# Optimization experiments

Measured on AMD Instinct MI355X. Metric: run time of the kernel, lower is better.

Reference implementation:

```python
import jax, jax.numpy as jnp
import numpy as np

SIDE = 9
STATE = SIDE * SIDE          # 81
NA = 5                       # stay, up, down, left, right
_MOVES = [(0, 0), (-1, 0), (1, 0), (0, -1), (0, 1)]

def _dest(s, a):
    r, c = divmod(s, SIDE)
    nr, nc = r + _MOVES[a][0], c + _MOVES[a][1]
    if 0 <= nr < SIDE and 0 <= nc < SIDE:
        return nr * SIDE + nc
    return s  # off-grid moves stay in place

# inflows[i] = all (s, a) with dest(s, a) == i; flattened as edge lists.
_src, _dst = [], []
for s in range(STATE):
    for a in range(NA):
        _src.append(s * NA + a)          # flat index into action_count[B, 81*5]
        _dst.append(_dest(s, a))
INFLOW_SRC = jnp.asarray(np.array(_src, dtype=np.int32))
INFLOW_DST = jnp.asarray(np.array(_dst, dtype=np.int32))


def setup_inputs() -> dict:
    key = jax.random.key(0)
    k1, k2, k3, k4, k5 = jax.random.split(key, 5)
    B = 131072
    obs = jax.random.uniform(k1, (B, 3 * STATE), dtype=jnp.float32)
    action_count = jax.random.uniform(k2, (B, STATE, NA), dtype=jnp.float32)
    W1 = jax.random.normal(k3, (STATE, 32), dtype=jnp.float32) * 0.1
    W2 = jax.random.normal(k4, (32, 32), dtype=jnp.float32) * 0.1
    W3 = jax.random.normal(k5, (32, 1), dtype=jnp.float32) * 0.1
    b3 = jnp.zeros((1,), dtype=jnp.float32)
    return {"obs": obs, "action_count": action_count,
            "W1": W1, "W2": W2, "W3": W3, "b3": b3}


def reference(obs, action_count, W1, W2, W3, b3):
    B = obs.shape[0]
    demand_count = obs[:, 2 * STATE:]                       # [B, 81]
    af = action_count.reshape(B, STATE * NA)                # [B, 405]
    # Vectorized replacement of the per-state gather+stack+reduce_sum loops:
    # next_state_count[b, i] = sum over (s,a) in inflows[i] of action_count[b, s, a]
    next_state_count = jnp.zeros((B, STATE), af.dtype).at[:, INFLOW_DST].add(af[:, INFLOW_SRC])
    # served_demand[b, i] = min(next_state_count[b, i], demand_count[b, i])
    served_demands = jnp.minimum(next_state_count, demand_count)
    immediate_reward = jnp.sum(served_demands, axis=1)      # [B]
    # value MLP on next_state_count (hidden dense layers have no bias)
    x = jax.nn.relu(next_state_count @ W1)
    x = jax.nn.relu(x @ W2)
    next_return = (x @ W3 + b3)[:, 0]                       # [B]
    symbolic_val = immediate_reward + next_return           # stack+reduce_sum
    return symbolic_val, immediate_reward, next_return, next_state_count
```

## Files before the change

kernel.cpp:

```cpp
#include <hip/hip_runtime.h>

#define SIDE 9
#define STATE 81
#define NA 5
#define NJ (STATE * NA)
#define H1 32
#define H2 32

struct DstTab { int v[NJ]; };
constexpr DstTab make_dst() {
    DstTab t{};
    const int dr[NA] = {0, -1, 1, 0, 0};
    const int dc[NA] = {0, 0, 0, -1, 1};
    for (int s = 0; s < STATE; ++s) {
        int r = s / SIDE, c = s % SIDE;
        for (int a = 0; a < NA; ++a) {
            int nr = r + dr[a], nc = c + dc[a];
            int d = (nr >= 0 && nr < SIDE && nc >= 0 && nc < SIDE) ? nr * SIDE + nc : s;
            t.v[s * NA + a] = d;
        }
    }
    return t;
}
constexpr DstTab DST = make_dst();

__global__ __launch_bounds__(256) void grid_vpn_kernel(
    const float* __restrict__ obs,
    const float* __restrict__ af,
    const float* __restrict__ W1,
    const float* __restrict__ W2,
    const float* __restrict__ W3,
    const float* __restrict__ b3,
    float* __restrict__ out,
    int B)
{
    int b = blockIdx.x * blockDim.x + threadIdx.x;
    if (b >= B) return;

    const float* afr = af + (size_t)b * NJ;
    float nsc[STATE];
#pragma unroll
    for (int d = 0; d < STATE; ++d) nsc[d] = 0.0f;
#pragma unroll
    for (int j = 0; j < NJ; ++j) {
        nsc[DST.v[j]] += afr[j];
    }

    const float* dem = obs + (size_t)b * (3 * STATE) + 2 * STATE;
    float ir = 0.0f;
#pragma unroll
    for (int d = 0; d < STATE; ++d) ir += fminf(nsc[d], dem[d]);

    float* nso = out + 3 * (size_t)B + (size_t)b * STATE;
#pragma unroll
    for (int d = 0; d < STATE; ++d) nso[d] = nsc[d];

    float x1[H1];
#pragma unroll
    for (int j = 0; j < H1; ++j) x1[j] = 0.0f;
#pragma unroll
    for (int d = 0; d < STATE; ++d) {
        float v = nsc[d];
#pragma unroll
        for (int j = 0; j < H1; ++j) x1[j] = fmaf(v, W1[d * H1 + j], x1[j]);
    }
#pragma unroll
    for (int j = 0; j < H1; ++j) x1[j] = fmaxf(x1[j], 0.0f);

    float x2[H2];
#pragma unroll
    for (int j = 0; j < H2; ++j) x2[j] = 0.0f;
#pragma unroll
    for (int k = 0; k < H1; ++k) {
        float v = x1[k];
#pragma unroll
        for (int j = 0; j < H2; ++j) x2[j] = fmaf(v, W2[k * H2 + j], x2[j]);
    }
#pragma unroll
    for (int j = 0; j < H2; ++j) x2[j] = fmaxf(x2[j], 0.0f);

    float nr = b3[0];
#pragma unroll
    for (int k = 0; k < H2; ++k) nr = fmaf(x2[k], W3[k], nr);

    out[b] = ir + nr;
    out[(size_t)B + b] = ir;
    out[2 * (size_t)B + b] = nr;
}

extern "C" void kernel_launch(void* const* d_in, const int* in_sizes, int n_in,
                              void* d_out, int out_size, void* d_ws, size_t ws_size,
                              hipStream_t stream) {
    const float* obs = (const float*)d_in[0];
    const float* ac  = (const float*)d_in[1];
    const float* W1  = (const float*)d_in[2];
    const float* W2  = (const float*)d_in[3];
    const float* W3  = (const float*)d_in[4];
    const float* b3  = (const float*)d_in[5];
    float* out = (float*)d_out;

    int B = in_sizes[0] / (3 * STATE);
    int block = 256;
    int grid = (B + block - 1) / block;
    hipLaunchKernelGGL(grid_vpn_kernel, dim3(grid), dim3(block), 0, stream,
                       obs, ac, W1, W2, W3, b3, out, B);
}
```

Before: 439.2 us.

## Stage row-strided inputs through LDS with async global_load_lds double buffering

Replaces the one-thread-per-row strided global loads with coalesced wave-wide global_load_lds copies of 27-column chunks into a double-buffered LDS tile, overlapping the next chunk's load with the scatter-add on the current one. The next_state_count output is also transposed through LDS so its stores are coalesced. Blocks shrink to a single 64-lane wave with launch_bounds(64,2). This relies on hand-written s_waitcnt counts and removes the sync barriers, which is fragile and may limit occupancy.

```diff
diff --git a/kernel.cpp b/kernel.cpp
--- a/kernel.cpp
+++ b/kernel.cpp
@@ -6,6 +6,11 @@
 #define NJ (STATE * NA)
 #define H1 32
 #define H2 32
+
+#define CCH 27
+#define ROWS 64
+#define NAF 15
+#define NCH 18
 
 struct DstTab { int v[NJ]; };
 constexpr DstTab make_dst() {
@@ -24,7 +29,10 @@
 }
 constexpr DstTab DST = make_dst();
 
-__global__ __launch_bounds__(256) void grid_vpn_kernel(
+typedef const float __attribute__((address_space(1)))* gas_fptr;
+typedef float __attribute__((address_space(3)))* las_fptr;
+
+__global__ __launch_bounds__(64, 2) void grid_vpn_kernel(
     const float* __restrict__ obs,
     const float* __restrict__ af,
     const float* __restrict__ W1,
@@ -34,26 +42,75 @@
     float* __restrict__ out,
     int B)
 {
-    int b = blockIdx.x * blockDim.x + threadIdx.x;
-    if (b >= B) return;
+    __shared__ float buf[2][ROWS * CCH];
+    const int lane = (int)threadIdx.x;
+    const int r0   = (int)blockIdx.x * ROWS;
+    const int Bm1  = B - 1;
 
-    const float* afr = af + (size_t)b * NJ;
+    const int lr0 = lane / CCH;
+    const int lc0 = lane - lr0 * CCH;
+
+    auto issue = [&](int c) {
+        const float* src = (c < NAF) ? af : obs;
+        const int stride = (c < NAF) ? NJ : 3 * STATE;
+        const int cb     = (c < NAF) ? c * CCH : 2 * STATE + (c - NAF) * CCH;
+        float* lb = &buf[c & 1][0];
+        int r = lr0, col = lc0;
+#pragma unroll
+        for (int t = 0; t < CCH; ++t) {
+            int rr = r0 + r; rr = (rr <= Bm1) ? rr : Bm1;
+            const float* gp = src + (size_t)rr * stride + (cb + col);
+            __builtin_amdgcn_global_load_lds((gas_fptr)gp, (las_fptr)(lb + t * 64), 4, 0, 0);
+            col += 64 - 2 * CCH;
+            int w = (col >= CCH) ? 1 : 0;
+            r += 2 + w;
+            col -= w ? CCH : 0;
+        }
+    };
+
     float nsc[STATE];
 #pragma unroll
     for (int d = 0; d < STATE; ++d) nsc[d] = 0.0f;
+    float ir = 0.0f;
+
+    issue(0);
+    issue(1);
 #pragma unroll
-    for (int j = 0; j < NJ; ++j) {
-        nsc[DST.v[j]] += afr[j];
+    for (int c = 0; c < NCH; ++c) {
+        if (c < NCH - 1) asm volatile("s_waitcnt vmcnt(27)" ::: "memory");
+        else             asm volatile("s_waitcnt vmcnt(0)"  ::: "memory");
+        const float* lb = &buf[c & 1][lane * CCH];
+        if (c < NAF) {
+#pragma unroll
+            for (int j0 = 0; j0 < CCH; ++j0)
+                nsc[DST.v[c * CCH + j0]] += lb[j0];
+        } else {
+#pragma unroll
+            for (int j0 = 0; j0 < CCH; ++j0)
+                ir += fminf(nsc[(c - NAF) * CCH + j0], lb[j0]);
+        }
+        asm volatile("s_waitcnt lgkmcnt(0)" ::: "memory");
+        if (c + 2 < NCH) issue(c + 2);
     }
 
-    const float* dem = obs + (size_t)b * (3 * STATE) + 2 * STATE;
-    float ir = 0.0f;
 #pragma unroll
-    for (int d = 0; d < STATE; ++d) ir += fminf(nsc[d], dem[d]);
-
-    float* nso = out + 3 * (size_t)B + (size_t)b * STATE;
+    for (int rc = 0; rc < 3; ++rc) {
+        float* lb = &buf[rc & 1][0];
 #pragma unroll
-    for (int d = 0; d < STATE; ++d) nso[d] = nsc[d];
+        for (int j0 = 0; j0 < CCH; ++j0)
+            lb[lane * CCH + j0] = nsc[rc * CCH + j0];
+        int r = lr0, col = lc0;
+#pragma unroll
+        for (int t = 0; t < CCH; ++t) {
+            int rr = r0 + r;
+            if (rr < B)
+                out[3 * (size_t)B + (size_t)rr * STATE + (rc * CCH + col)] = lb[t * 64 + lane];
+            col += 64 - 2 * CCH;
+            int w = (col >= CCH) ? 1 : 0;
+            r += 2 + w;
+            col -= w ? CCH : 0;
+        }
+    }
 
     float x1[H1];
 #pragma unroll
@@ -83,9 +140,12 @@
 #pragma unroll
     for (int k = 0; k < H2; ++k) nr = fmaf(x2[k], W3[k], nr);
 
-    out[b] = ir + nr;
-    out[(size_t)B + b] = ir;
-    out[2 * (size_t)B + b] = nr;
+    int b = r0 + lane;
+    if (b < B) {
+        out[b] = ir + nr;
+        out[(size_t)B + b] = ir;
+        out[2 * (size_t)B + b] = nr;
+    }
 }
 
 extern "C" void kernel_launch(void* const* d_in, const int* in_sizes, int n_in,
@@ -100,8 +160,8 @@
     float* out = (float*)d_out;
 
     int B = in_sizes[0] / (3 * STATE);
-    int block = 256;
-    int grid = (B + block - 1) / block;
+    int block = ROWS;
+    int grid = (B + ROWS - 1) / ROWS;
     hipLaunchKernelGGL(grid_vpn_kernel, dim3(grid), dim3(block), 0, stream,
                        obs, ac, W1, W2, W3, b3, out, B);
 }
```

Measured after the change: 495.4 us. 1.13x slower.

## Coalesce row loads and next-state stores through LDS staging with register prefetch

Applied to the files above, without the earlier changes.

Replaces per-thread strided row reads of action_count and demand with block-cooperative coalesced loads into shared memory. The data is staged in 27-column chunks, and the next chunk is prefetched into registers while the current one is consumed. The next_state_count output is transposed through LDS so global stores are coalesced, and launch bounds request 3 blocks per CU. The cost removed is uncoalesced memory traffic. In exchange it adds many barriers and extra LDS traffic, and the larger register footprint may hurt occupancy.

```diff
diff --git a/kernel.cpp b/kernel.cpp
--- a/kernel.cpp
+++ b/kernel.cpp
@@ -6,6 +6,12 @@
 #define NJ (STATE * NA)
 #define H1 32
 #define H2 32
+
+#define CCH 27
+#define BROWS 256
+#define NAF 15
+#define NCH 18
+#define OBS_STRIDE (3 * STATE)
 
 struct DstTab { int v[NJ]; };
 constexpr DstTab make_dst() {
@@ -24,7 +30,7 @@
 }
 constexpr DstTab DST = make_dst();
 
-__global__ __launch_bounds__(256) void grid_vpn_kernel(
+__global__ __launch_bounds__(256, 3) void grid_vpn_kernel(
     const float* __restrict__ obs,
     const float* __restrict__ af,
     const float* __restrict__ W1,
@@ -34,26 +40,79 @@
     float* __restrict__ out,
     int B)
 {
-    int b = blockIdx.x * blockDim.x + threadIdx.x;
-    if (b >= B) return;
+    __shared__ float lb[BROWS * CCH];
 
-    const float* afr = af + (size_t)b * NJ;
+    const int tid = (int)threadIdx.x;
+    const int r0  = (int)blockIdx.x * BROWS;
+    const int Bm1 = B - 1;
+
+    const int sr_r0 = tid / CCH;
+    const int sr_c0 = tid - sr_r0 * CCH;
+
     float nsc[STATE];
 #pragma unroll
     for (int d = 0; d < STATE; ++d) nsc[d] = 0.0f;
+    float ir = 0.0f;
+
+    float stg[CCH];
+
+    auto loadRegs = [&](int c, float (&s)[CCH]) {
+        const float* src = (c < NAF) ? af : obs;
+        const int stride = (c < NAF) ? NJ : OBS_STRIDE;
+        const int cb     = (c < NAF) ? c * CCH : 2 * STATE + (c - NAF) * CCH;
+        int r = sr_r0, col = sr_c0;
 #pragma unroll
-    for (int j = 0; j < NJ; ++j) {
-        nsc[DST.v[j]] += afr[j];
+        for (int t = 0; t < CCH; ++t) {
+            int rr = r0 + r; rr = (rr <= Bm1) ? rr : Bm1;
+            s[t] = src[(size_t)rr * stride + (cb + col)];
+            col += 256 - 9 * CCH;
+            int w = (col >= CCH) ? 1 : 0;
+            r += 9 + w;
+            col -= w ? CCH : 0;
+        }
+    };
+
+    loadRegs(0, stg);
+#pragma unroll
+    for (int c = 0; c < NCH; ++c) {
+#pragma unroll
+        for (int t = 0; t < CCH; ++t) lb[t * BROWS + tid] = stg[t];
+        if (c + 1 < NCH) loadRegs(c + 1, stg);
+        asm volatile("s_waitcnt lgkmcnt(0)" ::: "memory");
+        __builtin_amdgcn_s_barrier();
+        if (c < NAF) {
+#pragma unroll
+            for (int j = 0; j < CCH; ++j)
+                nsc[DST.v[c * CCH + j]] += lb[tid * CCH + j];
+        } else {
+#pragma unroll
+            for (int j = 0; j < CCH; ++j)
+                ir += fminf(nsc[(c - NAF) * CCH + j], lb[tid * CCH + j]);
+        }
+        asm volatile("s_waitcnt lgkmcnt(0)" ::: "memory");
+        __builtin_amdgcn_s_barrier();
     }
 
-    const float* dem = obs + (size_t)b * (3 * STATE) + 2 * STATE;
-    float ir = 0.0f;
+    {
+        const int wv = tid >> 6;
+        const int ln = tid & 63;
+        float* outns = out + 3 * (size_t)B + (size_t)r0 * STATE;
 #pragma unroll
-    for (int d = 0; d < STATE; ++d) ir += fminf(nsc[d], dem[d]);
-
-    float* nso = out + 3 * (size_t)B + (size_t)b * STATE;
+        for (int g = 0; g < 4; ++g) {
+            if (wv == g) {
 #pragma unroll
-    for (int d = 0; d < STATE; ++d) nso[d] = nsc[d];
+                for (int j = 0; j < STATE; ++j) lb[ln * STATE + j] = nsc[j];
+            }
+            asm volatile("s_waitcnt lgkmcnt(0)" ::: "memory");
+            __builtin_amdgcn_s_barrier();
+#pragma unroll
+            for (int t = 0; t < 20; ++t)
+                outns[g * 5184 + t * 256 + tid] = lb[t * 256 + tid];
+            if (tid < 64) outns[g * 5184 + 5120 + tid] = lb[5120 + tid];
+            asm volatile("s_waitcnt lgkmcnt(0)" ::: "memory");
+            __builtin_amdgcn_s_barrier();
+        }
+    }
 
     float x1[H1];
 #pragma unroll
@@ -83,9 +142,12 @@
 #pragma unroll
     for (int k = 0; k < H2; ++k) nr = fmaf(x2[k], W3[k], nr);
 
-    out[b] = ir + nr;
-    out[(size_t)B + b] = ir;
-    out[2 * (size_t)B + b] = nr;
+    int b = r0 + tid;
+    if (b < B) {
+        out[b] = ir + nr;
+        out[(size_t)B + b] = ir;
+        out[2 * (size_t)B + b] = nr;
+    }
 }
 
 extern "C" void kernel_launch(void* const* d_in, const int* in_sizes, int n_in,
@@ -100,8 +162,8 @@
     float* out = (float*)d_out;
 
     int B = in_sizes[0] / (3 * STATE);
-    int block = 256;
-    int grid = (B + block - 1) / block;
+    int block = BROWS;
+    int grid = (B + BROWS - 1) / BROWS;
     hipLaunchKernelGGL(grid_vpn_kernel, dim3(grid), dim3(block), 0, stream,
                        obs, ac, W1, W2, W3, b3, out, B);
 }
```

After: 428.5 us. 1.02x faster.
